# Performance work log

Hardware: AMD Instinct MI355X
Metric: run time of the kernel (lower is better)

Reference implementation:

```python
import jax, jax.numpy as jnp
import numpy as np

DIM = 512
HEADS = 16
HEAD_DIM = DIM // HEADS
SCALE = HEAD_DIM ** -0.5


def setup_inputs() -> dict:
    key = jax.random.key(0)
    k = jax.random.split(key, 6)
    B_, N = 2048, 49
    nW = 64
    x = jax.random.normal(k[0], (B_, N, DIM), dtype=jnp.float32)
    mask = jax.random.normal(k[1], (nW, N, N), dtype=jnp.float32)
    W_qkv = jax.random.normal(k[2], (3 * DIM, DIM), dtype=jnp.float32) * 0.02
    b_qkv = jnp.zeros((3 * DIM,), dtype=jnp.float32)
    W_proj = jax.random.normal(k[3], (DIM, DIM), dtype=jnp.float32) * 0.02
    b_proj = jnp.zeros((DIM,), dtype=jnp.float32)
    return {"x": x, "mask": mask, "W_qkv": W_qkv, "b_qkv": b_qkv,
            "W_proj": W_proj, "b_proj": b_proj}


def reference(x, mask, W_qkv, b_qkv, W_proj, b_proj):
    B_, N, C = x.shape
    H, d = HEADS, HEAD_DIM
    nW = mask.shape[0]
    # qkv projection: [B_, N, 3, H, d] -> q,k,v each [B_, H, N, d]
    qkv = (x @ W_qkv.T + b_qkv).reshape(B_, N, 3, H, d)
    qkv = jnp.transpose(qkv, (2, 0, 3, 1, 4))
    q, k, v = qkv[0], qkv[1], qkv[2]
    attn = jnp.einsum('bhnd,bhmd->bhnm', q * SCALE, k)  # [B_, H, N, N]
    # add per-window additive mask, broadcast over B_//nW groups and heads
    attn = attn.reshape(B_ // nW, nW, H, N, N) + mask[None, :, None, :, :]
    attn = attn.reshape(B_, H, N, N)
    attn = jax.nn.softmax(attn, axis=-1)
    out = jnp.einsum('bhnm,bhmd->bhnd', attn, v)  # [B_, H, N, d]
    out = jnp.transpose(out, (0, 2, 1, 3)).reshape(B_, N, C)
    return out @ W_proj.T + b_proj
```

## Files before the change

kernel.cpp:

```cpp
#include <hip/hip_runtime.h>


typedef unsigned short ushort_t;
typedef __bf16 bf16x8 __attribute__((ext_vector_type(8)));
typedef float f32x4 __attribute__((ext_vector_type(4)));
typedef unsigned short us8 __attribute__((ext_vector_type(8)));

#define SCALE_F 0.17677669529663687f
constexpr size_t QKV_REG = 2048ULL * 16 * 49 * 32;

__device__ __forceinline__ ushort_t f2bf(float f) {
  unsigned u = __builtin_bit_cast(unsigned, f);
  u += 0x7FFFu + ((u >> 16) & 1u);
  return (ushort_t)(u >> 16);
}

__device__ __forceinline__ void gload_lds16(const void* g, void* l) {
  __builtin_amdgcn_global_load_lds(
      (const __attribute__((address_space(1))) void*)g,
      (__attribute__((address_space(3))) void*)l, 16, 0, 0);
}

__global__ __launch_bounds__(256) void k_cvt(const float* __restrict__ in,
                                             ushort_t* __restrict__ out, int n4) {
  int i = blockIdx.x * blockDim.x + threadIdx.x;
  if (i >= n4) return;
  float4 v = reinterpret_cast<const float4*>(in)[i];
  ushort4 o = make_ushort4(f2bf(v.x), f2bf(v.y), f2bf(v.z), f2bf(v.w));
  reinterpret_cast<ushort4*>(out)[i] = o;
}

template <int EPI>
__global__ __launch_bounds__(256) void k_gemm(const ushort_t* __restrict__ A,
                                              const ushort_t* __restrict__ W,
                                              const float* __restrict__ bias,
                                              ushort_t* __restrict__ out_qkv,
                                              float* __restrict__ out_f,
                                              int nt_o) {
  __shared__ __align__(16) ushort_t As[128][64];
  __shared__ __align__(16) ushort_t Ws[128][64];

  const int tid  = threadIdx.x;
  const int lane = tid & 63;
  const int wv   = tid >> 6;
  const int wr   = wv >> 1, wc = wv & 1;

  const int cpx = gridDim.x >> 3;
  const int lid = (blockIdx.x & 7) * cpx + (blockIdx.x >> 3);
  const int bm  = lid / nt_o;
  const int bo  = lid - bm * nt_o;
  const size_t m0 = (size_t)bm * 128;
  const int o0    = bo * 128;

  f32x4 acc[4][4];
#pragma unroll
  for (int i = 0; i < 4; i++)
#pragma unroll
    for (int j = 0; j < 4; j++) acc[i][j] = f32x4{0.f, 0.f, 0.f, 0.f};

  const int srow   = wv * 32 + (lane >> 3);
  const int schunk = (((lane & 7) ^ (lane >> 3)) * 8);

  for (int kt = 0; kt < 8; ++kt) {
    const int k0 = kt * 64;
#pragma unroll
    for (int i = 0; i < 4; i++) {
      const ushort_t* g = A + (m0 + srow + i * 8) * 512 + k0 + schunk;
      gload_lds16(g, &As[wv * 32 + i * 8][0]);
    }
#pragma unroll
    for (int i = 0; i < 4; i++) {
      const ushort_t* g = W + (size_t)(o0 + srow + i * 8) * 512 + k0 + schunk;
      gload_lds16(g, &Ws[wv * 32 + i * 8][0]);
    }
    __syncthreads();
    const int fr = lane & 15;
#pragma unroll
    for (int kk = 0; kk < 2; ++kk) {
      const int ch = kk * 4 + (lane >> 4);
      const int cb = ((ch ^ (lane & 7)) << 3);
      uint4 ar[4], br[4];
#pragma unroll
      for (int mi = 0; mi < 4; mi++)
        ar[mi] = *reinterpret_cast<const uint4*>(&As[wr * 64 + mi * 16 + fr][cb]);
#pragma unroll
      for (int ni = 0; ni < 4; ni++)
        br[ni] = *reinterpret_cast<const uint4*>(&Ws[wc * 64 + ni * 16 + fr][cb]);
#pragma unroll
      for (int mi = 0; mi < 4; mi++)
#pragma unroll
        for (int ni = 0; ni < 4; ni++)
          acc[mi][ni] = __builtin_amdgcn_mfma_f32_16x16x32_bf16(
              __builtin_bit_cast(bf16x8, ar[mi]),
              __builtin_bit_cast(bf16x8, br[ni]), acc[mi][ni], 0, 0, 0);
    }
    __syncthreads();
  }

  const int colbase = lane & 15;
  const int rowgrp  = (lane >> 4) * 4;

  if constexpr (EPI == 1) {
#pragma unroll
    for (int ni = 0; ni < 4; ni++) {
      const int o = o0 + wc * 64 + ni * 16 + colbase;
      const float bv = bias[o];
#pragma unroll
      for (int mi = 0; mi < 4; mi++) {
        const size_t mrow = m0 + wr * 64 + mi * 16 + rowgrp;
#pragma unroll
        for (int r = 0; r < 4; r++)
          out_f[(mrow + r) * 512 + o] = acc[mi][ni][r] + bv;
      }
    }
  } else {
#pragma unroll
    for (int mi = 0; mi < 4; mi++) {
#pragma unroll
      for (int r = 0; r < 4; r++) {
        const int t = (int)m0 + wr * 64 + mi * 16 + rowgrp + r;
        const int b = t / 49;
        const int n = t - b * 49;
#pragma unroll
        for (int ni = 0; ni < 4; ni++) {
          const int o = o0 + wc * 64 + ni * 16 + colbase;
          const int which = o >> 9;
          const int h = (o >> 5) & 15;
          const int dd = o & 31;
          const size_t dst = (size_t)which * QKV_REG +
                             (((size_t)b * 16 + h) * 49 + n) * 32 + dd;
          out_qkv[dst] = f2bf(acc[mi][ni][r] + bias[o]);
        }
      }
    }
  }
}

__global__ __launch_bounds__(256) void k_attn(const ushort_t* __restrict__ qkv,
                                              const float* __restrict__ mask,
                                              ushort_t* __restrict__ aout) {
  __shared__ __align__(16) ushort_t Vt[32][64];
  __shared__ __align__(16) ushort_t Ps[4][16][64];

  const int tid  = threadIdx.x;
  const int lane = tid & 63;
  const int mt   = tid >> 6;
  const int bh   = blockIdx.x;
  const int b    = bh >> 4, h = bh & 15;
  const int w    = b & 63;
  const size_t base = (size_t)bh * (49 * 32);
  const ushort_t* qb = qkv + base;
  const ushort_t* kb = qkv + QKV_REG + base;
  const ushort_t* vb = qkv + 2 * QKV_REG + base;

  reinterpret_cast<uint4*>(&Vt[0][0])[tid] = make_uint4(0, 0, 0, 0);
  __syncthreads();
  if (tid < 196) {
    const int n = tid >> 2, d0 = (tid & 3) * 8;
    uint4 raw = *reinterpret_cast<const uint4*>(vb + n * 32 + d0);
    us8 e = __builtin_bit_cast(us8, raw);
#pragma unroll
    for (int j = 0; j < 8; j++) {
      Vt[d0 + j][(((n >> 3) ^ j) << 3) | (n & 7)] = e[j];
    }
  }
  __syncthreads();

  const int arow = lane & 15;
  const int kc   = (lane >> 4) * 8;

  uint4 qraw = *reinterpret_cast<const uint4*>(qb + (mt * 16 + arow) * 32 + kc);
  bf16x8 qa = __builtin_bit_cast(bf16x8, qraw);
  f32x4 s[4];
#pragma unroll
  for (int ni = 0; ni < 4; ni++) {
    uint4 kraw = *reinterpret_cast<const uint4*>(kb + (ni * 16 + arow) * 32 + kc);
    f32x4 z = {0.f, 0.f, 0.f, 0.f};
    s[ni] = __builtin_amdgcn_mfma_f32_16x16x32_bf16(
        qa, __builtin_bit_cast(bf16x8, kraw), z, 0, 0, 0);
  }

  const int rg = (lane >> 4) * 4;
  float rsum[4];
#pragma unroll
  for (int r = 0; r < 4; r++) {
    const int qr = mt * 16 + rg + r;
    float sv[4];
    float mx = -1e30f;
#pragma unroll
    for (int ni = 0; ni < 4; ni++) {
      const int col = ni * 16 + arow;
      float v;
      if (qr < 49 && col < 49)
        v = s[ni][r] * SCALE_F + mask[(size_t)w * 2401 + qr * 49 + col];
      else
        v = -1e30f;
      sv[ni] = v;
      mx = fmaxf(mx, v);
    }
#pragma unroll
    for (int off = 1; off < 16; off <<= 1) mx = fmaxf(mx, __shfl_xor(mx, off));
    float sum = 0.f;
    const int prow = rg + r;
#pragma unroll
    for (int ni = 0; ni < 4; ni++) {
      float p = __expf(sv[ni] - mx);
      sum += p;
      const int pcol = ni * 16 + arow;
      Ps[mt][prow][(((pcol >> 3) ^ (prow & 7)) << 3) | (pcol & 7)] = f2bf(p);
    }
#pragma unroll
    for (int off = 1; off < 16; off <<= 1) sum += __shfl_xor(sum, off);
    rsum[r] = sum;
  }

  __syncthreads();

  f32x4 o0 = {0.f, 0.f, 0.f, 0.f}, o1 = {0.f, 0.f, 0.f, 0.f};
#pragma unroll
  for (int kk = 0; kk < 2; kk++) {
    const int ch = kk * 4 + (lane >> 4);
    const int cb = ((ch ^ (lane & 7)) << 3);
    uint4 praw = *reinterpret_cast<const uint4*>(&Ps[mt][arow][cb]);
    bf16x8 pa = __builtin_bit_cast(bf16x8, praw);
    uint4 v0 = *reinterpret_cast<const uint4*>(&Vt[arow][cb]);
    uint4 v1 = *reinterpret_cast<const uint4*>(&Vt[16 + arow][cb]);
    o0 = __builtin_amdgcn_mfma_f32_16x16x32_bf16(pa, __builtin_bit_cast(bf16x8, v0), o0, 0, 0, 0);
    o1 = __builtin_amdgcn_mfma_f32_16x16x32_bf16(pa, __builtin_bit_cast(bf16x8, v1), o1, 0, 0, 0);
  }

#pragma unroll
  for (int r = 0; r < 4; r++) {
    const int qr = mt * 16 + rg + r;
    if (qr < 49) {
      const float inv = 1.f / rsum[r];
      aout[((size_t)b * 49 + qr) * 512 + h * 32 + arow]      = f2bf(o0[r] * inv);
      aout[((size_t)b * 49 + qr) * 512 + h * 32 + 16 + arow] = f2bf(o1[r] * inv);
    }
  }
}

extern "C" void kernel_launch(void* const* d_in, const int* in_sizes, int n_in,
                              void* d_out, int out_size, void* d_ws, size_t ws_size,
                              hipStream_t stream) {
  const float* x      = (const float*)d_in[0];
  const float* mask   = (const float*)d_in[1];
  const float* W_qkv  = (const float*)d_in[2];
  const float* b_qkv  = (const float*)d_in[3];
  const float* W_proj = (const float*)d_in[4];
  const float* b_proj = (const float*)d_in[5];
  float* out = (float*)d_out;

  ushort_t* ws     = (ushort_t*)d_ws;
  ushort_t* xb     = ws;
  ushort_t* qkvb   = ws + 51380224UL;
  ushort_t* aoutb  = ws + 205520896UL;
  ushort_t* wqkvb  = ws + 256901120UL;
  ushort_t* wprojb = ws + 257687552UL;

  const int n4x = 51380224 / 4, n4q = 786432 / 4, n4p = 262144 / 4;
  k_cvt<<<(n4x + 255) / 256, 256, 0, stream>>>(x, xb, n4x);
  k_cvt<<<(n4q + 255) / 256, 256, 0, stream>>>(W_qkv, wqkvb, n4q);
  k_cvt<<<(n4p + 255) / 256, 256, 0, stream>>>(W_proj, wprojb, n4p);

  k_gemm<0><<<784 * 12, 256, 0, stream>>>(xb, wqkvb, b_qkv, qkvb, nullptr, 12);

  k_attn<<<2048 * 16, 256, 0, stream>>>(qkvb, mask, aoutb);

  k_gemm<1><<<784 * 4, 256, 0, stream>>>(aoutb, wprojb, b_proj, nullptr, out, 4);
}
```

Measured before the change: 592.9 us.

## Rewrite GEMMs as 256x256 double-buffered 8-wave kernels with interleaved prefetch

```diff
diff --git a/kernel.cpp b/kernel.cpp
--- a/kernel.cpp
+++ b/kernel.cpp
@@ -31,99 +31,181 @@
 }
 
 template <int EPI>
-__global__ __launch_bounds__(256) void k_gemm(const ushort_t* __restrict__ A,
-                                              const ushort_t* __restrict__ W,
-                                              const float* __restrict__ bias,
-                                              ushort_t* __restrict__ out_qkv,
-                                              float* __restrict__ out_f,
-                                              int nt_o) {
-  __shared__ __align__(16) ushort_t As[128][64];
-  __shared__ __align__(16) ushort_t Ws[128][64];
+__global__ __launch_bounds__(512, 2) void k_gemm8(const ushort_t* __restrict__ A,
+                                                  const ushort_t* __restrict__ W,
+                                                  const float* __restrict__ bias,
+                                                  ushort_t* __restrict__ out_qkv,
+                                                  float* __restrict__ out_f,
+                                                  int nt_o) {
+  __shared__ __align__(16) ushort_t As[2][256][64];
+  __shared__ __align__(16) ushort_t Ws[2][256][64];
 
   const int tid  = threadIdx.x;
   const int lane = tid & 63;
   const int wv   = tid >> 6;
-  const int wr   = wv >> 1, wc = wv & 1;
+  const int wm   = wv >> 2, wn = wv & 3;
 
   const int cpx = gridDim.x >> 3;
   const int lid = (blockIdx.x & 7) * cpx + (blockIdx.x >> 3);
   const int bm  = lid / nt_o;
   const int bo  = lid - bm * nt_o;
-  const size_t m0 = (size_t)bm * 128;
-  const int o0    = bo * 128;
-
-  f32x4 acc[4][4];
-#pragma unroll
-  for (int i = 0; i < 4; i++)
+  const size_t m0 = (size_t)bm * 256;
+  const int o0    = bo * 256;
+
+  const int seg0 = wv * 2;
+  const int srow = seg0 * 8 + (lane >> 3);
+  const int scol = ((lane & 7) ^ (lane >> 3)) * 8;
+  const ushort_t* Ag = A + (m0 + srow) * 512 + scol;
+  const ushort_t* Wg = W + (size_t)(o0 + srow) * 512 + scol;
+
+  auto stageA = [&](int bb, int h, int kt) {
+    const ushort_t* g = Ag + (size_t)h * (128 * 512) + kt * 64;
+    gload_lds16(g,           &As[bb][h * 128 + seg0 * 8][0]);
+    gload_lds16(g + 8 * 512, &As[bb][h * 128 + seg0 * 8 + 8][0]);
+  };
+  auto stageW = [&](int bb, int h, int kt) {
+    const ushort_t* g = Wg + (size_t)h * (128 * 512) + kt * 64;
+    gload_lds16(g,           &Ws[bb][h * 128 + seg0 * 8][0]);
+    gload_lds16(g + 8 * 512, &Ws[bb][h * 128 + seg0 * 8 + 8][0]);
+  };
+
+  const int fr  = lane & 15;
+  const int cb0 = lane >> 4;
+  auto readA = [&](int bb, int mi, int kk) -> uint4 {
+    const int row = wm * 128 + mi * 16 + fr;
+    const int ch  = (kk * 4 + cb0) ^ (fr & 7);
+    return *reinterpret_cast<const uint4*>(&As[bb][row][ch * 8]);
+  };
+  auto readW = [&](int bb, int ni, int kk) -> uint4 {
+    const int row = wn * 64 + ni * 16 + fr;
+    const int ch  = (kk * 4 + cb0) ^ (fr & 7);
+    return *reinterpret_cast<const uint4*>(&Ws[bb][row][ch * 8]);
+  };
+  auto MF = [&](uint4 a, uint4 b, f32x4 c) -> f32x4 {
+    return __builtin_amdgcn_mfma_f32_16x16x32_bf16(
+        __builtin_bit_cast(bf16x8, a), __builtin_bit_cast(bf16x8, b), c, 0, 0, 0);
+  };
+
+  f32x4 acc[8][4];
+#pragma unroll
+  for (int i = 0; i < 8; i++)
 #pragma unroll
     for (int j = 0; j < 4; j++) acc[i][j] = f32x4{0.f, 0.f, 0.f, 0.f};
 
-  const int srow   = wv * 32 + (lane >> 3);
-  const int schunk = (((lane & 7) ^ (lane >> 3)) * 8);
-
-  for (int kt = 0; kt < 8; ++kt) {
-    const int k0 = kt * 64;
-#pragma unroll
-    for (int i = 0; i < 4; i++) {
-      const ushort_t* g = A + (m0 + srow + i * 8) * 512 + k0 + schunk;
-      gload_lds16(g, &As[wv * 32 + i * 8][0]);
-    }
-#pragma unroll
-    for (int i = 0; i < 4; i++) {
-      const ushort_t* g = W + (size_t)(o0 + srow + i * 8) * 512 + k0 + schunk;
-      gload_lds16(g, &Ws[wv * 32 + i * 8][0]);
-    }
-    __syncthreads();
-    const int fr = lane & 15;
-#pragma unroll
-    for (int kk = 0; kk < 2; ++kk) {
-      const int ch = kk * 4 + (lane >> 4);
-      const int cb = ((ch ^ (lane & 7)) << 3);
-      uint4 ar[4], br[4];
-#pragma unroll
-      for (int mi = 0; mi < 4; mi++)
-        ar[mi] = *reinterpret_cast<const uint4*>(&As[wr * 64 + mi * 16 + fr][cb]);
-#pragma unroll
-      for (int ni = 0; ni < 4; ni++)
-        br[ni] = *reinterpret_cast<const uint4*>(&Ws[wc * 64 + ni * 16 + fr][cb]);
-#pragma unroll
-      for (int mi = 0; mi < 4; mi++)
-#pragma unroll
-        for (int ni = 0; ni < 4; ni++)
-          acc[mi][ni] = __builtin_amdgcn_mfma_f32_16x16x32_bf16(
-              __builtin_bit_cast(bf16x8, ar[mi]),
-              __builtin_bit_cast(bf16x8, br[ni]), acc[mi][ni], 0, 0, 0);
-    }
-    __syncthreads();
-  }
+  uint4 am[4][2], bn[4][2];
+
+  stageA(0, 0, 0); stageA(0, 1, 0); stageW(0, 0, 0); stageW(0, 1, 0);
+  stageW(1, 0, 1); stageW(1, 1, 1); stageA(1, 0, 1);
+  asm volatile("s_waitcnt vmcnt(6)" ::: "memory");
+  __builtin_amdgcn_s_barrier();
+
+  for (int t = 0; t < 8; t += 2) {
+#pragma unroll
+    for (int hf = 0; hf < 2; ++hf) {
+      const int bb  = hf;
+      const int tt  = t + hf;
+      const int kt1 = (tt + 1 < 8) ? (tt + 1) : 7;
+      const int kt2 = (tt + 2 < 8) ? (tt + 2) : 7;
+
+#pragma unroll
+      for (int j = 0; j < 4; ++j)
+#pragma unroll
+        for (int kk = 0; kk < 2; ++kk) am[j][kk] = readA(bb, j, kk);
+#pragma unroll
+      for (int ni = 0; ni < 2; ++ni)
+#pragma unroll
+        for (int kk = 0; kk < 2; ++kk) bn[ni][kk] = readW(bb, ni, kk);
+      stageA(bb ^ 1, 1, kt1);
+      __builtin_amdgcn_s_barrier();
+      __builtin_amdgcn_s_setprio(1);
+#pragma unroll
+      for (int j = 0; j < 4; ++j)
+#pragma unroll
+        for (int ni = 0; ni < 2; ++ni)
+#pragma unroll
+          for (int kk = 0; kk < 2; ++kk)
+            acc[j][ni] = MF(am[j][kk], bn[ni][kk], acc[j][ni]);
+      __builtin_amdgcn_s_setprio(0);
+      __builtin_amdgcn_s_barrier();
+
+#pragma unroll
+      for (int ni = 2; ni < 4; ++ni)
+#pragma unroll
+        for (int kk = 0; kk < 2; ++kk) bn[ni][kk] = readW(bb, ni, kk);
+      __builtin_amdgcn_s_barrier();
+      __builtin_amdgcn_s_setprio(1);
+#pragma unroll
+      for (int j = 0; j < 4; ++j)
+#pragma unroll
+        for (int ni = 2; ni < 4; ++ni)
+#pragma unroll
+          for (int kk = 0; kk < 2; ++kk)
+            acc[j][ni] = MF(am[j][kk], bn[ni][kk], acc[j][ni]);
+      __builtin_amdgcn_s_setprio(0);
+      __builtin_amdgcn_s_barrier();
+
+#pragma unroll
+      for (int j = 0; j < 4; ++j)
+#pragma unroll
+        for (int kk = 0; kk < 2; ++kk) am[j][kk] = readA(bb, 4 + j, kk);
+      stageW(bb, 0, kt2);
+      __builtin_amdgcn_s_barrier();
+      __builtin_amdgcn_s_setprio(1);
+#pragma unroll
+      for (int j = 0; j < 4; ++j)
+#pragma unroll
+        for (int ni = 0; ni < 2; ++ni)
+#pragma unroll
+          for (int kk = 0; kk < 2; ++kk)
+            acc[4 + j][ni] = MF(am[j][kk], bn[ni][kk], acc[4 + j][ni]);
+      __builtin_amdgcn_s_setprio(0);
+      __builtin_amdgcn_s_barrier();
+
+      stageA(bb, 0, kt2);
+      stageW(bb, 1, kt2);
+      __builtin_amdgcn_s_barrier();
+      __builtin_amdgcn_s_setprio(1);
+#pragma unroll
+      for (int j = 0; j < 4; ++j)
+#pragma unroll
+        for (int ni = 2; ni < 4; ++ni)
+#pragma unroll
+          for (int kk = 0; kk < 2; ++kk)
+            acc[4 + j][ni] = MF(am[j][kk], bn[ni][kk], acc[4 + j][ni]);
+      __builtin_amdgcn_s_setprio(0);
+      asm volatile("s_waitcnt vmcnt(6)" ::: "memory");
+      __builtin_amdgcn_s_barrier();
+    }
+  }
+  asm volatile("s_waitcnt vmcnt(0)" ::: "memory");
 
   const int colbase = lane & 15;
-  const int rowgrp  = (lane >> 4) * 4;
+  const int rg      = (lane >> 4) * 4;
 
   if constexpr (EPI == 1) {
 #pragma unroll
-    for (int ni = 0; ni < 4; ni++) {
-      const int o = o0 + wc * 64 + ni * 16 + colbase;
+    for (int ni = 0; ni < 4; ++ni) {
+      const int o = o0 + wn * 64 + ni * 16 + colbase;
       const float bv = bias[o];
 #pragma unroll
-      for (int mi = 0; mi < 4; mi++) {
-        const size_t mrow = m0 + wr * 64 + mi * 16 + rowgrp;
-#pragma unroll
-        for (int r = 0; r < 4; r++)
+      for (int mi = 0; mi < 8; ++mi) {
+        const size_t mrow = m0 + wm * 128 + mi * 16 + rg;
+#pragma unroll
+        for (int r = 0; r < 4; ++r)
           out_f[(mrow + r) * 512 + o] = acc[mi][ni][r] + bv;
       }
     }
   } else {
 #pragma unroll
-    for (int mi = 0; mi < 4; mi++) {
-#pragma unroll
-      for (int r = 0; r < 4; r++) {
-        const int t = (int)m0 + wr * 64 + mi * 16 + rowgrp + r;
-        const int b = t / 49;
-        const int n = t - b * 49;
-#pragma unroll
-        for (int ni = 0; ni < 4; ni++) {
-          const int o = o0 + wc * 64 + ni * 16 + colbase;
+    for (int mi = 0; mi < 8; ++mi) {
+#pragma unroll
+      for (int r = 0; r < 4; ++r) {
+        const int tkn = (int)m0 + wm * 128 + mi * 16 + rg + r;
+        const int b = tkn / 49;
+        const int n = tkn - b * 49;
+#pragma unroll
+        for (int ni = 0; ni < 4; ++ni) {
+          const int o = o0 + wn * 64 + ni * 16 + colbase;
           const int which = o >> 9;
           const int h = (o >> 5) & 15;
           const int dd = o & 31;
@@ -160,9 +242,8 @@
     uint4 raw = *reinterpret_cast<const uint4*>(vb + n * 32 + d0);
     us8 e = __builtin_bit_cast(us8, raw);
 #pragma unroll
-    for (int j = 0; j < 8; j++) {
+    for (int j = 0; j < 8; j++)
       Vt[d0 + j][(((n >> 3) ^ j) << 3) | (n & 7)] = e[j];
-    }
   }
   __syncthreads();
 
@@ -263,9 +344,9 @@
   k_cvt<<<(n4q + 255) / 256, 256, 0, stream>>>(W_qkv, wqkvb, n4q);
   k_cvt<<<(n4p + 255) / 256, 256, 0, stream>>>(W_proj, wprojb, n4p);
 
-  k_gemm<0><<<784 * 12, 256, 0, stream>>>(xb, wqkvb, b_qkv, qkvb, nullptr, 12);
+  k_gemm8<0><<<392 * 6, 512, 0, stream>>>(xb, wqkvb, b_qkv, qkvb, nullptr, 6);
 
   k_attn<<<2048 * 16, 256, 0, stream>>>(qkvb, mask, aoutb);
 
-  k_gemm<1><<<784 * 4, 256, 0, stream>>>(aoutb, wprojb, b_proj, nullptr, out, 4);
-}
+  k_gemm8<1><<<392 * 2, 512, 0, stream>>>(aoutb, wprojb, b_proj, nullptr, out, 2);
+}
```

New measurement: 626.9 us. +5.7%, slower.

## Fuse fp32-to-bf16 conversion of x into the QKV GEMM A-tile load

Applied to the files above, without the earlier changes.

```diff
diff --git a/kernel.cpp b/kernel.cpp
--- a/kernel.cpp
+++ b/kernel.cpp
@@ -13,6 +13,15 @@
   unsigned u = __builtin_bit_cast(unsigned, f);
   u += 0x7FFFu + ((u >> 16) & 1u);
   return (ushort_t)(u >> 16);
+}
+
+__device__ __forceinline__ uint4 pack8(float4 a, float4 b) {
+  uint4 r;
+  r.x = (unsigned)f2bf(a.x) | ((unsigned)f2bf(a.y) << 16);
+  r.y = (unsigned)f2bf(a.z) | ((unsigned)f2bf(a.w) << 16);
+  r.z = (unsigned)f2bf(b.x) | ((unsigned)f2bf(b.y) << 16);
+  r.w = (unsigned)f2bf(b.z) | ((unsigned)f2bf(b.w) << 16);
+  return r;
 }
 
 __device__ __forceinline__ void gload_lds16(const void* g, void* l) {
@@ -30,15 +39,13 @@
   reinterpret_cast<ushort4*>(out)[i] = o;
 }
 
-template <int EPI>
-__global__ __launch_bounds__(256) void k_gemm(const ushort_t* __restrict__ A,
-                                              const ushort_t* __restrict__ W,
-                                              const float* __restrict__ bias,
-                                              ushort_t* __restrict__ out_qkv,
-                                              float* __restrict__ out_f,
-                                              int nt_o) {
+__global__ __launch_bounds__(256) void k_gemm1f(const float* __restrict__ X,
+                                                const ushort_t* __restrict__ W,
+                                                const float* __restrict__ bias,
+                                                ushort_t* __restrict__ out_qkv) {
   __shared__ __align__(16) ushort_t As[128][64];
   __shared__ __align__(16) ushort_t Ws[128][64];
+  constexpr int nt_o = 12;
 
   const int tid  = threadIdx.x;
   const int lane = tid & 63;
@@ -58,22 +65,42 @@
 #pragma unroll
     for (int j = 0; j < 4; j++) acc[i][j] = f32x4{0.f, 0.f, 0.f, 0.f};
 
-  const int srow   = wv * 32 + (lane >> 3);
-  const int schunk = (((lane & 7) ^ (lane >> 3)) * 8);
-
+  const int arow0 = wv * 32 + (lane >> 3);
+  const int acol  = (lane & 7) * 8;
+  const int aswc  = ((lane & 7) ^ (lane >> 3)) * 8;
+  const float* Xg = X + (m0 + arow0) * 512 + acol;
+
+  const ushort_t* Wg = W + (size_t)(o0 + arow0) * 512 + (size_t)aswc;
+
+  auto loadA = [&](int kt, float4 (&ar)[4][2]) {
+#pragma unroll
+    for (int i = 0; i < 4; i++) {
+      const float* g = Xg + (size_t)i * (8 * 512) + kt * 64;
+      ar[i][0] = *reinterpret_cast<const float4*>(g);
+      ar[i][1] = *reinterpret_cast<const float4*>(g + 4);
+    }
+  };
+  auto writeA = [&](const float4 (&ar)[4][2]) {
+#pragma unroll
+    for (int i = 0; i < 4; i++) {
+      uint4 p = pack8(ar[i][0], ar[i][1]);
+      *reinterpret_cast<uint4*>(&As[arow0 + i * 8][aswc]) = p;
+    }
+  };
+
+  float4 areg[2][4][2];
+  loadA(0, areg[0]);
+
+#pragma unroll
   for (int kt = 0; kt < 8; ++kt) {
-    const int k0 = kt * 64;
-#pragma unroll
-    for (int i = 0; i < 4; i++) {
-      const ushort_t* g = A + (m0 + srow + i * 8) * 512 + k0 + schunk;
-      gload_lds16(g, &As[wv * 32 + i * 8][0]);
-    }
-#pragma unroll
-    for (int i = 0; i < 4; i++) {
-      const ushort_t* g = W + (size_t)(o0 + srow + i * 8) * 512 + k0 + schunk;
-      gload_lds16(g, &Ws[wv * 32 + i * 8][0]);
-    }
+#pragma unroll
+    for (int i = 0; i < 4; i++)
+      gload_lds16(Wg + (size_t)i * (8 * 512) + kt * 64, &Ws[wv * 32 + i * 8][0]);
+    writeA(areg[kt & 1]);
     __syncthreads();
+
+    if (kt < 7) loadA(kt + 1, areg[(kt + 1) & 1]);
+
     const int fr = lane & 15;
 #pragma unroll
     for (int kk = 0; kk < 2; ++kk) {
@@ -99,39 +126,102 @@
 
   const int colbase = lane & 15;
   const int rowgrp  = (lane >> 4) * 4;
-
-  if constexpr (EPI == 1) {
-#pragma unroll
-    for (int ni = 0; ni < 4; ni++) {
-      const int o = o0 + wc * 64 + ni * 16 + colbase;
-      const float bv = bias[o];
-#pragma unroll
-      for (int mi = 0; mi < 4; mi++) {
-        const size_t mrow = m0 + wr * 64 + mi * 16 + rowgrp;
-#pragma unroll
-        for (int r = 0; r < 4; r++)
-          out_f[(mrow + r) * 512 + o] = acc[mi][ni][r] + bv;
+#pragma unroll
+  for (int mi = 0; mi < 4; mi++) {
+#pragma unroll
+    for (int r = 0; r < 4; r++) {
+      const int t = (int)m0 + wr * 64 + mi * 16 + rowgrp + r;
+      const int b = t / 49;
+      const int n = t - b * 49;
+#pragma unroll
+      for (int ni = 0; ni < 4; ni++) {
+        const int o = o0 + wc * 64 + ni * 16 + colbase;
+        const int which = o >> 9;
+        const int h = (o >> 5) & 15;
+        const int dd = o & 31;
+        const size_t dst = (size_t)which * QKV_REG +
+                           (((size_t)b * 16 + h) * 49 + n) * 32 + dd;
+        out_qkv[dst] = f2bf(acc[mi][ni][r] + bias[o]);
       }
     }
-  } else {
+  }
+}
+
+__global__ __launch_bounds__(256) void k_gemmB(const ushort_t* __restrict__ A,
+                                               const ushort_t* __restrict__ W,
+                                               const float* __restrict__ bias,
+                                               float* __restrict__ out_f,
+                                               int nt_o) {
+  __shared__ __align__(16) ushort_t As[128][64];
+  __shared__ __align__(16) ushort_t Ws[128][64];
+
+  const int tid  = threadIdx.x;
+  const int lane = tid & 63;
+  const int wv   = tid >> 6;
+  const int wr   = wv >> 1, wc = wv & 1;
+
+  const int cpx = gridDim.x >> 3;
+  const int lid = (blockIdx.x & 7) * cpx + (blockIdx.x >> 3);
+  const int bm  = lid / nt_o;
+  const int bo  = lid - bm * nt_o;
+  const size_t m0 = (size_t)bm * 128;
+  const int o0    = bo * 128;
+
+  f32x4 acc[4][4];
+#pragma unroll
+  for (int i = 0; i < 4; i++)
+#pragma unroll
+    for (int j = 0; j < 4; j++) acc[i][j] = f32x4{0.f, 0.f, 0.f, 0.f};
+
+  const int srow   = wv * 32 + (lane >> 3);
+  const int schunk = (((lane & 7) ^ (lane >> 3)) * 8);
+
+  for (int kt = 0; kt < 8; ++kt) {
+    const int k0 = kt * 64;
+#pragma unroll
+    for (int i = 0; i < 4; i++)
+      gload_lds16(A + (m0 + srow + i * 8) * 512 + k0 + schunk,
+                  &As[wv * 32 + i * 8][0]);
+#pragma unroll
+    for (int i = 0; i < 4; i++)
+      gload_lds16(W + (size_t)(o0 + srow + i * 8) * 512 + k0 + schunk,
+                  &Ws[wv * 32 + i * 8][0]);
+    __syncthreads();
+    const int fr = lane & 15;
+#pragma unroll
+    for (int kk = 0; kk < 2; ++kk) {
+      const int ch = kk * 4 + (lane >> 4);
+      const int cb = ((ch ^ (lane & 7)) << 3);
+      uint4 ar[4], br[4];
+#pragma unroll
+      for (int mi = 0; mi < 4; mi++)
+        ar[mi] = *reinterpret_cast<const uint4*>(&As[wr * 64 + mi * 16 + fr][cb]);
+#pragma unroll
+      for (int ni = 0; ni < 4; ni++)
+        br[ni] = *reinterpret_cast<const uint4*>(&Ws[wc * 64 + ni * 16 + fr][cb]);
+#pragma unroll
+      for (int mi = 0; mi < 4; mi++)
+#pragma unroll
+        for (int ni = 0; ni < 4; ni++)
+          acc[mi][ni] = __builtin_amdgcn_mfma_f32_16x16x32_bf16(
+              __builtin_bit_cast(bf16x8, ar[mi]),
+              __builtin_bit_cast(bf16x8, br[ni]), acc[mi][ni], 0, 0, 0);
+    }
+    __syncthreads();
+  }
+
+  const int colbase = lane & 15;
+  const int rowgrp  = (lane >> 4) * 4;
+#pragma unroll
+  for (int ni = 0; ni < 4; ni++) {
+    const int o = o0 + wc * 64 + ni * 16 + colbase;
+    const float bv = bias[o];
 #pragma unroll
     for (int mi = 0; mi < 4; mi++) {
-#pragma unroll
-      for (int r = 0; r < 4; r++) {
-        const int t = (int)m0 + wr * 64 + mi * 16 + rowgrp + r;
-        const int b = t / 49;
-        const int n = t - b * 49;
-#pragma unroll
-        for (int ni = 0; ni < 4; ni++) {
-          const int o = o0 + wc * 64 + ni * 16 + colbase;
-          const int which = o >> 9;
-          const int h = (o >> 5) & 15;
-          const int dd = o & 31;
-          const size_t dst = (size_t)which * QKV_REG +
-                             (((size_t)b * 16 + h) * 49 + n) * 32 + dd;
-          out_qkv[dst] = f2bf(acc[mi][ni][r] + bias[o]);
-        }
-      }
+      const size_t mrow = m0 + wr * 64 + mi * 16 + rowgrp;
+#pragma unroll
+      for (int r = 0; r < 4; r++)
+        out_f[(mrow + r) * 512 + o] = acc[mi][ni][r] + bv;
     }
   }
 }
@@ -160,9 +250,8 @@
     uint4 raw = *reinterpret_cast<const uint4*>(vb + n * 32 + d0);
     us8 e = __builtin_bit_cast(us8, raw);
 #pragma unroll
-    for (int j = 0; j < 8; j++) {
+    for (int j = 0; j < 8; j++)
       Vt[d0 + j][(((n >> 3) ^ j) << 3) | (n & 7)] = e[j];
-    }
   }
   __syncthreads();
 
@@ -252,20 +341,18 @@
   float* out = (float*)d_out;
 
   ushort_t* ws     = (ushort_t*)d_ws;
-  ushort_t* xb     = ws;
-  ushort_t* qkvb   = ws + 51380224UL;
-  ushort_t* aoutb  = ws + 205520896UL;
-  ushort_t* wqkvb  = ws + 256901120UL;
-  ushort_t* wprojb = ws + 257687552UL;
-
-  const int n4x = 51380224 / 4, n4q = 786432 / 4, n4p = 262144 / 4;
-  k_cvt<<<(n4x + 255) / 256, 256, 0, stream>>>(x, xb, n4x);
+  ushort_t* qkvb   = ws;
+  ushort_t* aoutb  = ws + 154140672UL;
+  ushort_t* wqkvb  = ws + 205520896UL;
+  ushort_t* wprojb = ws + 206307328UL;
+
+  const int n4q = 786432 / 4, n4p = 262144 / 4;
   k_cvt<<<(n4q + 255) / 256, 256, 0, stream>>>(W_qkv, wqkvb, n4q);
   k_cvt<<<(n4p + 255) / 256, 256, 0, stream>>>(W_proj, wprojb, n4p);
 
-  k_gemm<0><<<784 * 12, 256, 0, stream>>>(xb, wqkvb, b_qkv, qkvb, nullptr, 12);
+  k_gemm1f<<<784 * 12, 256, 0, stream>>>(x, wqkvb, b_qkv, qkvb);
 
   k_attn<<<2048 * 16, 256, 0, stream>>>(qkvb, mask, aoutb);
 
-  k_gemm<1><<<784 * 4, 256, 0, stream>>>(aoutb, wprojb, b_proj, nullptr, out, 4);
-}
+  k_gemmB<<<784 * 4, 256, 0, stream>>>(aoutb, wprojb, b_proj, out, 4);
+}
```

Measured after the change: 713.5 us. 20.3% more time.

## Double-buffer GEMM LDS tiles to overlap global loads with MFMA compute

Applied to the files above, without the earlier changes.

```diff
diff --git a/kernel.cpp b/kernel.cpp
--- a/kernel.cpp
+++ b/kernel.cpp
@@ -31,14 +31,14 @@
 }
 
 template <int EPI>
-__global__ __launch_bounds__(256) void k_gemm(const ushort_t* __restrict__ A,
-                                              const ushort_t* __restrict__ W,
-                                              const float* __restrict__ bias,
-                                              ushort_t* __restrict__ out_qkv,
-                                              float* __restrict__ out_f,
-                                              int nt_o) {
-  __shared__ __align__(16) ushort_t As[128][64];
-  __shared__ __align__(16) ushort_t Ws[128][64];
+__global__ __launch_bounds__(256) void k_gemmP(const ushort_t* __restrict__ A,
+                                               const ushort_t* __restrict__ W,
+                                               const float* __restrict__ bias,
+                                               ushort_t* __restrict__ out_qkv,
+                                               float* __restrict__ out_f,
+                                               int nt_o) {
+  __shared__ __align__(16) ushort_t As[2][128][64];
+  __shared__ __align__(16) ushort_t Ws[2][128][64];
 
   const int tid  = threadIdx.x;
   const int lane = tid & 63;
@@ -60,21 +60,20 @@
 
   const int srow   = wv * 32 + (lane >> 3);
   const int schunk = (((lane & 7) ^ (lane >> 3)) * 8);
-
-  for (int kt = 0; kt < 8; ++kt) {
-    const int k0 = kt * 64;
-#pragma unroll
-    for (int i = 0; i < 4; i++) {
-      const ushort_t* g = A + (m0 + srow + i * 8) * 512 + k0 + schunk;
-      gload_lds16(g, &As[wv * 32 + i * 8][0]);
-    }
-#pragma unroll
-    for (int i = 0; i < 4; i++) {
-      const ushort_t* g = W + (size_t)(o0 + srow + i * 8) * 512 + k0 + schunk;
-      gload_lds16(g, &Ws[wv * 32 + i * 8][0]);
-    }
-    __syncthreads();
-    const int fr = lane & 15;
+  const ushort_t* Ags = A + (m0 + srow) * 512 + schunk;
+  const ushort_t* Wgs = W + (size_t)(o0 + srow) * 512 + schunk;
+
+  auto stage = [&](int kt, int bb) {
+#pragma unroll
+    for (int i = 0; i < 4; i++)
+      gload_lds16(Ags + (size_t)i * (8 * 512) + kt * 64, &As[bb][wv * 32 + i * 8][0]);
+#pragma unroll
+    for (int i = 0; i < 4; i++)
+      gload_lds16(Wgs + (size_t)i * (8 * 512) + kt * 64, &Ws[bb][wv * 32 + i * 8][0]);
+  };
+
+  const int fr = lane & 15;
+  auto compute = [&](int bb) {
 #pragma unroll
     for (int kk = 0; kk < 2; ++kk) {
       const int ch = kk * 4 + (lane >> 4);
@@ -82,10 +81,10 @@
       uint4 ar[4], br[4];
 #pragma unroll
       for (int mi = 0; mi < 4; mi++)
-        ar[mi] = *reinterpret_cast<const uint4*>(&As[wr * 64 + mi * 16 + fr][cb]);
+        ar[mi] = *reinterpret_cast<const uint4*>(&As[bb][wr * 64 + mi * 16 + fr][cb]);
 #pragma unroll
       for (int ni = 0; ni < 4; ni++)
-        br[ni] = *reinterpret_cast<const uint4*>(&Ws[wc * 64 + ni * 16 + fr][cb]);
+        br[ni] = *reinterpret_cast<const uint4*>(&Ws[bb][wc * 64 + ni * 16 + fr][cb]);
 #pragma unroll
       for (int mi = 0; mi < 4; mi++)
 #pragma unroll
@@ -94,8 +93,24 @@
               __builtin_bit_cast(bf16x8, ar[mi]),
               __builtin_bit_cast(bf16x8, br[ni]), acc[mi][ni], 0, 0, 0);
     }
-    __syncthreads();
-  }
+  };
+
+  stage(0, 0);
+  stage(1, 1);
+
+  for (int kt = 0; kt < 7; ++kt) {
+    asm volatile("s_waitcnt vmcnt(8)" ::: "memory");
+    __builtin_amdgcn_s_barrier();
+    __builtin_amdgcn_sched_barrier(0);
+    compute(kt & 1);
+    __builtin_amdgcn_sched_barrier(0);
+    __builtin_amdgcn_s_barrier();
+    if (kt < 6) stage(kt + 2, kt & 1);
+  }
+  asm volatile("s_waitcnt vmcnt(0)" ::: "memory");
+  __builtin_amdgcn_s_barrier();
+  __builtin_amdgcn_sched_barrier(0);
+  compute(1);
 
   const int colbase = lane & 15;
   const int rowgrp  = (lane >> 4) * 4;
@@ -160,9 +175,8 @@
     uint4 raw = *reinterpret_cast<const uint4*>(vb + n * 32 + d0);
     us8 e = __builtin_bit_cast(us8, raw);
 #pragma unroll
-    for (int j = 0; j < 8; j++) {
+    for (int j = 0; j < 8; j++)
       Vt[d0 + j][(((n >> 3) ^ j) << 3) | (n & 7)] = e[j];
-    }
   }
   __syncthreads();
 
@@ -263,9 +277,9 @@
   k_cvt<<<(n4q + 255) / 256, 256, 0, stream>>>(W_qkv, wqkvb, n4q);
   k_cvt<<<(n4p + 255) / 256, 256, 0, stream>>>(W_proj, wprojb, n4p);
 
-  k_gemm<0><<<784 * 12, 256, 0, stream>>>(xb, wqkvb, b_qkv, qkvb, nullptr, 12);
+  k_gemmP<0><<<784 * 12, 256, 0, stream>>>(xb, wqkvb, b_qkv, qkvb, nullptr, 12);
 
   k_attn<<<2048 * 16, 256, 0, stream>>>(qkvb, mask, aoutb);
 
-  k_gemm<1><<<784 * 4, 256, 0, stream>>>(aoutb, wprojb, b_proj, nullptr, out, 4);
-}
+  k_gemmP<1><<<784 * 4, 256, 0, stream>>>(aoutb, wprojb, b_proj, nullptr, out, 4);
+}
```

Result: no change. 601.7 us (+1.5%).
